# Kernel optimization log

Measured on AMD Instinct MI355X. Metric: run time of the kernel, lower is better.

## Reference

```python
import jax, jax.numpy as jnp
import numpy as np

K = 50  # top-k causal instances (UC_MIL constructor)


def setup_inputs() -> dict:
    key = jax.random.key(0)
    k1, k2 = jax.random.split(key)
    X = jax.random.normal(k1, (8, 4096, 768), dtype=jnp.float32)
    # GCN layer weight: nn.Linear(768, 1, bias=False) -> weight shape (1, 768)
    W = jax.random.normal(k2, (1, 768), dtype=jnp.float32) * 0.02
    return {"X": X, "W": W}


def reference(X, W):
    # X: (B, N, D) bag of instance features; W: (1, D) GCN weight
    B, N, D = X.shape
    k = K

    # --- build_adjacency_matrix, batched ---
    Xc = X - X.mean(axis=1, keepdims=True)                      # center over instances
    cov = jnp.einsum('bnd,bmd->bnm', Xc, Xc)                    # (B, N, N)
    var = jnp.sqrt(jnp.sum(Xc * Xc, axis=-1, keepdims=True)) + 1e-6  # (B, N, 1)
    corr = cov / (var * jnp.swapaxes(var, 1, 2))                # var @ var.T
    A = jnp.abs(corr)
    dinv = jnp.sum(A, axis=-1) ** (-0.5)                        # (B, N)
    # D @ A @ D with diagonal D == row/col scaling (same math, no dense diag)
    A_norm = dinv[:, :, None] * A * dinv[:, None, :]

    # --- 1-layer GCN score: (A_norm @ (X W^T)).squeeze(-1) ---
    XW = jnp.einsum('bnd,d->bn', X, W[0])                       # (B, N)
    S = jnp.einsum('bnm,bm->bn', A_norm, XW)                    # (B, N)

    # --- top-k causal / non-causal split, vectorized over batch ---
    _, topk_idx = jax.lax.top_k(S, k)                           # (B, k)
    F_c = jnp.take_along_axis(X, topk_idx[:, :, None], axis=1)  # (B, k, D)

    # non-topk indices in ascending order (torch.arange(N)[mask] semantics)
    flag = jnp.zeros((B, N), dtype=jnp.int32)
    flag = flag.at[jnp.arange(B)[:, None], topk_idx].set(1)
    non_idx = jnp.argsort(flag, axis=1, stable=True)[:, : N - k]  # (B, N-k)
    F_nc = jnp.take_along_axis(X, non_idx[:, :, None], axis=1)    # (B, N-k, D)

    # NOTE: original code has a bug: topk_indices = torch.stack(F_i_c, 0),
    # i.e. the second output is the gathered features, not the indices.
    # We replicate that faithfully.
    return (S,
            F_c,
            F_c.mean(axis=1, keepdims=True),
            F_nc.mean(axis=1, keepdims=True))
```

## Files before the change

kernel.cpp:

```cpp
#include <hip/hip_runtime.h>
#include <stdint.h>

typedef unsigned short u16;
typedef short bf16x8 __attribute__((ext_vector_type(8)));
typedef float f32x4 __attribute__((ext_vector_type(4)));
typedef unsigned long long ull;

#define NB 8
#define NROW 4096
#define ND 768
#define NKB 24
#define NRB 32
#define KTILE 4096
#define NTRI 528
#define TOPK 50

#define CPART_OFF 0u
#define CSUM_OFF  786432u
#define MEAN_OFF  811008u
#define RV_OFF    835584u
#define XW_OFF    966656u
#define T_OFF     1097728u
#define U_OFF     1228800u
#define DINV_OFF  1359872u
#define W_OFF     1490944u
#define IDX_OFF   1622016u
#define SMALL_TOTAL 1626112u
#define HB_PER_BATCH  6291456ull
#define COV_PER_BATCH 34603008ull
#define PER_BATCH (2ull * HB_PER_BATCH + COV_PER_BATCH)

static __device__ __forceinline__ u16 f2bf(float f) {
  uint32_t u = __float_as_uint(f);
  u += 0x7FFFu + ((u >> 16) & 1u);
  return (u16)(u >> 16);
}
static __device__ __forceinline__ float bf2f(u16 h) {
  return __uint_as_float(((uint32_t)h) << 16);
}

static __device__ __forceinline__ int tile_swz(int t) {
  return (t & 7) * 66 + (t >> 3);
}

__global__ __launch_bounds__(256)
void colsum1_kernel(const float* __restrict__ X, float* __restrict__ part) {
  const int nc = blockIdx.x;
  const int d  = threadIdx.x + blockIdx.y * 256;
  const int b  = blockIdx.z;
  const float* p = X + ((size_t)b * NROW + (size_t)nc * 128) * ND + d;
  float s = 0.f;
  for (int i = 0; i < 128; ++i) s += p[(size_t)i * ND];
  part[((size_t)b * 32 + nc) * ND + d] = s;
}

__global__ __launch_bounds__(256)
void colsum2_kernel(const float* __restrict__ part, float* __restrict__ csum,
                    float* __restrict__ mean) {
  const int d = threadIdx.x + blockIdx.x * 256;
  const int b = blockIdx.y;
  float s = 0.f;
  for (int i = 0; i < 32; ++i) s += part[((size_t)b * 32 + i) * ND + d];
  csum[(size_t)b * ND + d] = s;
  mean[(size_t)b * ND + d] = s * (1.0f / 4096.0f);
}

__global__ __launch_bounds__(128)
void rowstats_kernel(const float* __restrict__ X, const float* __restrict__ W,
                     const float* __restrict__ mean,
                     u16* __restrict__ hi, u16* __restrict__ lo,
                     float* __restrict__ rv, float* __restrict__ xw, int b0) {
  const int n  = blockIdx.x;
  const int lb = blockIdx.y;
  const int gb = b0 + lb;
  const int tid = threadIdx.x;
  const float* xr = X + ((size_t)gb * NROW + n) * ND;
  const float* mb = mean + (size_t)gb * ND;
  const int r = n & 127, rbk = n >> 7;
  float ssq = 0.f, sw = 0.f;
  if (tid < 96) {
    const int d0 = tid * 8;
    const float4 xa = *(const float4*)(xr + d0);
    const float4 xb = *(const float4*)(xr + d0 + 4);
    const float4 ma = *(const float4*)(mb + d0);
    const float4 mc = *(const float4*)(mb + d0 + 4);
    const float4 wa = *(const float4*)(W + d0);
    const float4 wb = *(const float4*)(W + d0 + 4);
    float x[8]  = {xa.x, xa.y, xa.z, xa.w, xb.x, xb.y, xb.z, xb.w};
    float mm[8] = {ma.x, ma.y, ma.z, ma.w, mc.x, mc.y, mc.z, mc.w};
    float ww[8] = {wa.x, wa.y, wa.z, wa.w, wb.x, wb.y, wb.z, wb.w};
    u16 hbits[8], lbits[8];
#pragma unroll
    for (int i = 0; i < 8; ++i) {
      float xc = x[i] - mm[i];
      ssq += xc * xc;
      sw  += x[i] * ww[i];
      u16 hb = f2bf(xc);
      float hf = bf2f(hb);
      u16 lb2 = f2bf(xc - hf);
      hbits[i] = hb; lbits[i] = lb2;
    }
    const int kb = d0 >> 5;
    const int kk = d0 & 31;
    const size_t tbyte = ((size_t)((lb * NRB + rbk) * NKB + kb)) * 8192
                       + (size_t)((r * 64 + kk * 2) ^ ((r & 7) << 4));
    uint4 hv, lv;
    hv.x = (uint32_t)hbits[0] | ((uint32_t)hbits[1] << 16);
    hv.y = (uint32_t)hbits[2] | ((uint32_t)hbits[3] << 16);
    hv.z = (uint32_t)hbits[4] | ((uint32_t)hbits[5] << 16);
    hv.w = (uint32_t)hbits[6] | ((uint32_t)hbits[7] << 16);
    lv.x = (uint32_t)lbits[0] | ((uint32_t)lbits[1] << 16);
    lv.y = (uint32_t)lbits[2] | ((uint32_t)lbits[3] << 16);
    lv.z = (uint32_t)lbits[4] | ((uint32_t)lbits[5] << 16);
    lv.w = (uint32_t)lbits[6] | ((uint32_t)lbits[7] << 16);
    *(uint4*)((char*)hi + tbyte) = hv;
    *(uint4*)((char*)lo + tbyte) = lv;
  }
#pragma unroll
  for (int m = 1; m < 64; m <<= 1) {
    ssq += __shfl_xor(ssq, m, 64);
    sw  += __shfl_xor(sw, m, 64);
  }
  __shared__ float sh[4];
  const int w = tid >> 6, lane = tid & 63;
  if (lane == 0) { sh[w * 2] = ssq; sh[w * 2 + 1] = sw; }
  __syncthreads();
  if (tid == 0) {
    float S = sh[0] + sh[2];
    float T = sh[1] + sh[3];
    const size_t i = (size_t)gb * NROW + n;
    rv[i] = 1.0f / (sqrtf(S) + 1e-6f);
    xw[i] = T;
  }
}

static __device__ __forceinline__ bf16x8 read_frag(const u16* sm, int r, int kbyte) {
  const int byte = (r * 64 + kbyte) ^ ((r & 7) << 4);
  return *(const bf16x8*)((const char*)sm + byte);
}

#define LOADK(kb)  do { const size_t kb8 = (size_t)(kb) * 8192;            \
  rA0 = *(const uint4*)(hA + kb8 + o0);  rA1 = *(const uint4*)(hA + kb8 + o1); \
  rB0 = *(const uint4*)(hB + kb8 + o0);  rB1 = *(const uint4*)(hB + kb8 + o1); \
  rLA0 = *(const uint4*)(lA + kb8 + o0); rLA1 = *(const uint4*)(lA + kb8 + o1); \
  rLB0 = *(const uint4*)(lB + kb8 + o0); rLB1 = *(const uint4*)(lB + kb8 + o1); } while (0)

__global__ __launch_bounds__(256, 2)
void gemm_acc_kernel(const u16* __restrict__ hi, const u16* __restrict__ lo,
                     const float* __restrict__ coef, float* __restrict__ outacc,
                     float* __restrict__ covout, int b0) {
  const int lb = blockIdx.y;
  const int gb = b0 + lb;
  const int tsw = tile_swz(blockIdx.x);
  int trem = tsw;
  int rb = 0;
  while (trem >= NRB - rb) { trem -= NRB - rb; ++rb; }
  const int cb = rb + trem;

  __shared__ u16 sm[4 * KTILE];
  u16* aHi = sm;
  u16* bHi = sm + KTILE;
  u16* aLo = sm + 2 * KTILE;
  u16* bLo = sm + 3 * KTILE;

  const int tid = threadIdx.x;
  const int lane = tid & 63;
  const int wid = tid >> 6;
  const int wrow = wid >> 1, wcol = wid & 1;
  const int l15 = lane & 15, lg = lane >> 4;

  const char* hA = (const char*)(hi + (size_t)((lb * NRB + rb) * NKB) * KTILE);
  const char* hB = (const char*)(hi + (size_t)((lb * NRB + cb) * NKB) * KTILE);
  const char* lA = (const char*)(lo + (size_t)((lb * NRB + rb) * NKB) * KTILE);
  const char* lB = (const char*)(lo + (size_t)((lb * NRB + cb) * NKB) * KTILE);

  const int o0 = tid * 16;
  const int o1 = o0 + 4096;

  uint4 rA0, rA1, rB0, rB1, rLA0, rLA1, rLB0, rLB1;

  f32x4 acc[4][4];
#pragma unroll
  for (int i = 0; i < 4; ++i)
#pragma unroll
    for (int j = 0; j < 4; ++j) acc[i][j] = f32x4{0.f, 0.f, 0.f, 0.f};

  LOADK(0);
  for (int kb = 0; kb < NKB; ++kb) {
    __syncthreads();
    *(uint4*)((char*)aHi + o0) = rA0;  *(uint4*)((char*)aHi + o1) = rA1;
    *(uint4*)((char*)bHi + o0) = rB0;  *(uint4*)((char*)bHi + o1) = rB1;
    *(uint4*)((char*)aLo + o0) = rLA0; *(uint4*)((char*)aLo + o1) = rLA1;
    *(uint4*)((char*)bLo + o0) = rLB0; *(uint4*)((char*)bLo + o1) = rLB1;
    __syncthreads();
    if (kb + 1 < NKB) { LOADK(kb + 1); }

    bf16x8 ah[4], bh[4], al[4], bl[4];
#pragma unroll
    for (int i = 0; i < 4; ++i) {
      ah[i] = read_frag(aHi, wrow * 64 + i * 16 + l15, lg * 16);
      bh[i] = read_frag(bHi, wcol * 64 + i * 16 + l15, lg * 16);
      al[i] = read_frag(aLo, wrow * 64 + i * 16 + l15, lg * 16);
      bl[i] = read_frag(bLo, wcol * 64 + i * 16 + l15, lg * 16);
    }
#pragma unroll
    for (int mi = 0; mi < 4; ++mi)
#pragma unroll
      for (int ni = 0; ni < 4; ++ni) {
        acc[mi][ni] = __builtin_amdgcn_mfma_f32_16x16x32_bf16(ah[mi], bh[ni], acc[mi][ni], 0, 0, 0);
        acc[mi][ni] = __builtin_amdgcn_mfma_f32_16x16x32_bf16(ah[mi], bl[ni], acc[mi][ni], 0, 0, 0);
        acc[mi][ni] = __builtin_amdgcn_mfma_f32_16x16x32_bf16(al[mi], bh[ni], acc[mi][ni], 0, 0, 0);
      }
  }

  const float* cf = coef + (size_t)gb * NROW;
  float* oa = outacc + (size_t)gb * NROW;
  const int rbase = rb * 128 + wrow * 64;
  const int cbase = cb * 128 + wcol * 64;

  float* cv = covout + ((size_t)lb * NTRI + tsw) * 16384;
#pragma unroll
  for (int mi = 0; mi < 4; ++mi)
#pragma unroll
    for (int ni = 0; ni < 4; ++ni)
#pragma unroll
      for (int j = 0; j < 4; ++j)
        cv[(wrow * 64 + mi * 16 + lg * 4 + j) * 128 + wcol * 64 + ni * 16 + l15] =
            fabsf(acc[mi][ni][j]);

  float ccol[4];
#pragma unroll
  for (int ni = 0; ni < 4; ++ni) ccol[ni] = cf[cbase + ni * 16 + l15];

  float rs[4][4];
#pragma unroll
  for (int mi = 0; mi < 4; ++mi)
#pragma unroll
    for (int j = 0; j < 4; ++j) {
      float s = 0.f;
#pragma unroll
      for (int ni = 0; ni < 4; ++ni) s += fabsf(acc[mi][ni][j]) * ccol[ni];
      rs[mi][j] = s;
    }
#pragma unroll
  for (int m = 1; m < 16; m <<= 1)
#pragma unroll
    for (int mi = 0; mi < 4; ++mi)
#pragma unroll
      for (int j = 0; j < 4; ++j) rs[mi][j] += __shfl_xor(rs[mi][j], m, 64);
  if (l15 == 0) {
#pragma unroll
    for (int mi = 0; mi < 4; ++mi)
#pragma unroll
      for (int j = 0; j < 4; ++j)
        atomicAdd(&oa[rbase + mi * 16 + lg * 4 + j], rs[mi][j]);
  }

  if (rb != cb) {
    float crow[4][4];
#pragma unroll
    for (int mi = 0; mi < 4; ++mi)
#pragma unroll
      for (int j = 0; j < 4; ++j) crow[mi][j] = cf[rbase + mi * 16 + lg * 4 + j];
    float cs[4];
#pragma unroll
    for (int ni = 0; ni < 4; ++ni) {
      float s = 0.f;
#pragma unroll
      for (int mi = 0; mi < 4; ++mi)
#pragma unroll
        for (int j = 0; j < 4; ++j) s += fabsf(acc[mi][ni][j]) * crow[mi][j];
      cs[ni] = s;
    }
#pragma unroll
    for (int ni = 0; ni < 4; ++ni) {
      cs[ni] += __shfl_xor(cs[ni], 16, 64);
      cs[ni] += __shfl_xor(cs[ni], 32, 64);
    }
    if (lg == 0) {
#pragma unroll
      for (int ni = 0; ni < 4; ++ni)
        atomicAdd(&oa[cbase + ni * 16 + l15], cs[ni]);
    }
  }
}

__global__ __launch_bounds__(256)
void upass_kernel(const float* __restrict__ cov, const float* __restrict__ w,
                  float* __restrict__ uacc, int b0) {
  const int lb = blockIdx.y;
  const int gb = b0 + lb;
  const int tsw = tile_swz(blockIdx.x);
  int trem = tsw;
  int rb = 0;
  while (trem >= NRB - rb) { trem -= NRB - rb; ++rb; }
  const int cb = rb + trem;

  const float* A = cov + ((size_t)lb * NTRI + tsw) * 16384;
  const float* wb_ = w + (size_t)gb * NROW;

  __shared__ float wr[128];
  __shared__ float rsum[128];
  __shared__ float csum_p[8][128];

  const int t = threadIdx.x;
  const int g = t >> 5;
  const int l = t & 31;

  if (t < 128) wr[t] = wb_[rb * 128 + t];
  const float4 wc4 = *(const float4*)(wb_ + cb * 128 + l * 4);
  __syncthreads();

  float sc0 = 0.f, sc1 = 0.f, sc2 = 0.f, sc3 = 0.f;
#pragma unroll
  for (int i = 0; i < 16; ++i) {
    const int r = g + i * 8;
    const float4 v = *(const float4*)(A + r * 128 + l * 4);
    float p = v.x * wc4.x + v.y * wc4.y + v.z * wc4.z + v.w * wc4.w;
    const float wrr = wr[r];
    sc0 += v.x * wrr; sc1 += v.y * wrr; sc2 += v.z * wrr; sc3 += v.w * wrr;
#pragma unroll
    for (int m = 1; m < 32; m <<= 1) p += __shfl_xor(p, m, 64);
    if (l == 0) rsum[r] = p;
  }
  csum_p[g][l * 4 + 0] = sc0;
  csum_p[g][l * 4 + 1] = sc1;
  csum_p[g][l * 4 + 2] = sc2;
  csum_p[g][l * 4 + 3] = sc3;
  __syncthreads();

  float* ua = uacc + (size_t)gb * NROW;
  if (t < 128) atomicAdd(&ua[rb * 128 + t], rsum[t]);
  if (rb != cb && t < 128) {
    float s = 0.f;
#pragma unroll
    for (int gg = 0; gg < 8; ++gg) s += csum_p[gg][t];
    atomicAdd(&ua[cb * 128 + t], s);
  }
}

__global__ __launch_bounds__(256)
void dinvw_kernel(const float* __restrict__ t, const float* __restrict__ rv,
                  const float* __restrict__ xw, float* __restrict__ dinv,
                  float* __restrict__ w, int b0) {
  const int n = blockIdx.x * 256 + threadIdx.x;
  const int gb = b0 + blockIdx.y;
  const size_t i = (size_t)gb * NROW + n;
  const float dv = 1.0f / sqrtf(rv[i] * t[i]);
  dinv[i] = dv;
  w[i] = dv * xw[i] * rv[i];
}

__global__ __launch_bounds__(256)
void sfinal_kernel(const float* __restrict__ dinv, const float* __restrict__ rv,
                   const float* __restrict__ u, float* __restrict__ S) {
  const int n = blockIdx.x * 256 + threadIdx.x;
  const int b = blockIdx.y;
  const size_t i = (size_t)b * NROW + n;
  S[i] = dinv[i] * rv[i] * u[i];
}

__global__ __launch_bounds__(1024)
void topk_kernel(const float* __restrict__ S, int* __restrict__ idx) {
  const int b = blockIdx.x;
  __shared__ ull keys[NROW];
  __shared__ ull wred[16];
  const int t = threadIdx.x;
  const int lane = t & 63, w = t >> 6;
  for (int i = t; i < NROW; i += 1024) {
    float s = S[(size_t)b * NROW + i];
    uint32_t u = __float_as_uint(s);
    u = (u & 0x80000000u) ? ~u : (u | 0x80000000u);
    keys[i] = ((ull)u << 32) | (uint32_t)(4095 - i);
  }
  __syncthreads();
  for (int r = 0; r < TOPK; ++r) {
    ull m = keys[t];
    ull m2 = keys[t + 1024]; if (m2 > m) m = m2;
    m2 = keys[t + 2048]; if (m2 > m) m = m2;
    m2 = keys[t + 3072]; if (m2 > m) m = m2;
#pragma unroll
    for (int sh = 1; sh < 64; sh <<= 1) {
      ull o = __shfl_xor(m, sh, 64);
      if (o > m) m = o;
    }
    if (lane == 0) wred[w] = m;
    __syncthreads();
    if (w == 0) {
      ull mm = wred[lane & 15];
#pragma unroll
      for (int sh = 1; sh < 16; sh <<= 1) {
        ull o = __shfl_xor(mm, sh, 64);
        if (o > mm) mm = o;
      }
      if (lane == 0) {
        const int sel = 4095 - (int)(mm & 0xFFFFFFFFu);
        idx[b * TOPK + r] = sel;
        keys[sel] = 0ULL;
      }
    }
    __syncthreads();
  }
}

__global__ __launch_bounds__(256)
void gather_kernel(const float* __restrict__ X, const int* __restrict__ idx,
                   float* __restrict__ outFc) {
  const int rr = blockIdx.x;
  const int b = blockIdx.y;
  const int row = idx[b * TOPK + rr];
  const float* src = X + ((size_t)b * NROW + row) * ND;
  float* dst = outFc + ((size_t)b * TOPK + rr) * ND;
#pragma unroll
  for (int c = 0; c < 3; ++c) {
    const int d = threadIdx.x + c * 256;
    dst[d] = src[d];
  }
}

__global__ __launch_bounds__(256)
void means_kernel(const float* __restrict__ X, const int* __restrict__ idx,
                  const float* __restrict__ csum, float* __restrict__ outC,
                  float* __restrict__ outNC) {
  const int b = blockIdx.x;
#pragma unroll
  for (int c = 0; c < 3; ++c) {
    const int d = threadIdx.x + c * 256;
    float s = 0.f;
    for (int r = 0; r < TOPK; ++r) {
      const int row = idx[b * TOPK + r];
      s += X[((size_t)b * NROW + row) * ND + d];
    }
    outC[(size_t)b * ND + d]  = s * (1.0f / 50.0f);
    outNC[(size_t)b * ND + d] = (csum[(size_t)b * ND + d] - s) * (1.0f / 4046.0f);
  }
}

extern "C" void kernel_launch(void* const* d_in, const int* in_sizes, int n_in,
                              void* d_out, int out_size, void* d_ws, size_t ws_size,
                              hipStream_t stream) {
  const float* X = (const float*)d_in[0];
  const float* W = (const float*)d_in[1];
  float* out = (float*)d_out;
  char* ws = (char*)d_ws;

  float* cpart = (float*)(ws + CPART_OFF);
  float* csum  = (float*)(ws + CSUM_OFF);
  float* mean  = (float*)(ws + MEAN_OFF);
  float* rv    = (float*)(ws + RV_OFF);
  float* xw    = (float*)(ws + XW_OFF);
  float* tacc  = (float*)(ws + T_OFF);
  float* uacc  = (float*)(ws + U_OFF);
  float* dinv  = (float*)(ws + DINV_OFF);
  float* warr  = (float*)(ws + W_OFF);
  int*   idx   = (int*)(ws + IDX_OFF);

  int nbc = 1;
  if (ws_size > SMALL_TOTAL + PER_BATCH)
    nbc = (int)((ws_size - SMALL_TOTAL) / PER_BATCH);
  if (nbc > NB) nbc = NB;
  if (nbc < 1) nbc = 1;
  u16* hi   = (u16*)(ws + SMALL_TOTAL);
  u16* lo   = (u16*)(ws + SMALL_TOTAL + (size_t)nbc * HB_PER_BATCH);
  float* cov = (float*)(ws + SMALL_TOTAL + (size_t)nbc * 2 * HB_PER_BATCH);

  float* outS  = out;
  float* outFc = out + 32768;
  float* outMC = out + 339968;
  float* outMN = out + 346112;

  hipMemsetAsync(ws + T_OFF, 0, 262144, stream);

  colsum1_kernel<<<dim3(32, 3, NB), 256, 0, stream>>>(X, cpart);
  colsum2_kernel<<<dim3(3, NB), 256, 0, stream>>>(cpart, csum, mean);

  for (int b0 = 0; b0 < NB; b0 += nbc) {
    const int nb = (NB - b0 < nbc) ? (NB - b0) : nbc;
    rowstats_kernel<<<dim3(NROW, nb), 128, 0, stream>>>(X, W, mean, hi, lo, rv, xw, b0);
    gemm_acc_kernel<<<dim3(NTRI, nb), 256, 0, stream>>>(hi, lo, rv, tacc, cov, b0);
    dinvw_kernel<<<dim3(16, nb), 256, 0, stream>>>(tacc, rv, xw, dinv, warr, b0);
    upass_kernel<<<dim3(NTRI, nb), 256, 0, stream>>>(cov, warr, uacc, b0);
  }

  sfinal_kernel<<<dim3(16, NB), 256, 0, stream>>>(dinv, rv, uacc, outS);
  topk_kernel<<<NB, 1024, 0, stream>>>(outS, idx);
  gather_kernel<<<dim3(TOPK, NB), 256, 0, stream>>>(X, idx, outFc);
  means_kernel<<<NB, 256, 0, stream>>>(X, idx, csum, outMC, outMN);
}
```

Baseline: 517.7 us.

## Double-buffer GEMM LDS tiles and fuse small elementwise and gather kernels

The GEMM kernel now uses two LDS buffers, issuing the next K-block's global loads before the MFMAs and storing them after, so each iteration needs one barrier instead of two. The dinv/w, S-final, gather and means kernels are removed: their math is recomputed inline in upass and topk, and gather plus means become one kernel. This cuts launch count and intermediate traffic. The cost is LDS doubling to 64KB per block, which may hurt the two-blocks-per-CU occupancy, plus redundant sqrt work in upass.

```diff
diff --git a/kernel.cpp b/kernel.cpp
--- a/kernel.cpp
+++ b/kernel.cpp
@@ -22,10 +22,8 @@
 #define XW_OFF    966656u
 #define T_OFF     1097728u
 #define U_OFF     1228800u
-#define DINV_OFF  1359872u
-#define W_OFF     1490944u
-#define IDX_OFF   1622016u
-#define SMALL_TOTAL 1626112u
+#define IDX_OFF   1359872u
+#define SMALL_TOTAL 1363968u
 #define HB_PER_BATCH  6291456ull
 #define COV_PER_BATCH 34603008ull
 #define PER_BATCH (2ull * HB_PER_BATCH + COV_PER_BATCH)
@@ -145,6 +143,12 @@
   rLA0 = *(const uint4*)(lA + kb8 + o0); rLA1 = *(const uint4*)(lA + kb8 + o1); \
   rLB0 = *(const uint4*)(lB + kb8 + o0); rLB1 = *(const uint4*)(lB + kb8 + o1); } while (0)
 
+#define STOREK(buf) do { char* bp = (char*)(buf);                          \
+  *(uint4*)(bp + o0) = rA0;          *(uint4*)(bp + o1) = rA1;             \
+  *(uint4*)(bp + 8192 + o0) = rB0;   *(uint4*)(bp + 8192 + o1) = rB1;      \
+  *(uint4*)(bp + 16384 + o0) = rLA0; *(uint4*)(bp + 16384 + o1) = rLA1;    \
+  *(uint4*)(bp + 24576 + o0) = rLB0; *(uint4*)(bp + 24576 + o1) = rLB1; } while (0)
+
 __global__ __launch_bounds__(256, 2)
 void gemm_acc_kernel(const u16* __restrict__ hi, const u16* __restrict__ lo,
                      const float* __restrict__ coef, float* __restrict__ outacc,
@@ -157,11 +161,7 @@
   while (trem >= NRB - rb) { trem -= NRB - rb; ++rb; }
   const int cb = rb + trem;
 
-  __shared__ u16 sm[4 * KTILE];
-  u16* aHi = sm;
-  u16* bHi = sm + KTILE;
-  u16* aLo = sm + 2 * KTILE;
-  u16* bLo = sm + 3 * KTILE;
+  __shared__ u16 sm[2][4 * KTILE];
 
   const int tid = threadIdx.x;
   const int lane = tid & 63;
@@ -186,14 +186,15 @@
     for (int j = 0; j < 4; ++j) acc[i][j] = f32x4{0.f, 0.f, 0.f, 0.f};
 
   LOADK(0);
+  STOREK(sm[0]);
+  __syncthreads();
+
+  int cur = 0;
   for (int kb = 0; kb < NKB; ++kb) {
-    __syncthreads();
-    *(uint4*)((char*)aHi + o0) = rA0;  *(uint4*)((char*)aHi + o1) = rA1;
-    *(uint4*)((char*)bHi + o0) = rB0;  *(uint4*)((char*)bHi + o1) = rB1;
-    *(uint4*)((char*)aLo + o0) = rLA0; *(uint4*)((char*)aLo + o1) = rLA1;
-    *(uint4*)((char*)bLo + o0) = rLB0; *(uint4*)((char*)bLo + o1) = rLB1;
-    __syncthreads();
-    if (kb + 1 < NKB) { LOADK(kb + 1); }
+    const u16* aHi = sm[cur];
+    const u16* bHi = sm[cur] + KTILE;
+    const u16* aLo = sm[cur] + 2 * KTILE;
+    const u16* bLo = sm[cur] + 3 * KTILE;
 
     bf16x8 ah[4], bh[4], al[4], bl[4];
 #pragma unroll
@@ -203,6 +204,8 @@
       al[i] = read_frag(aLo, wrow * 64 + i * 16 + l15, lg * 16);
       bl[i] = read_frag(bLo, wcol * 64 + i * 16 + l15, lg * 16);
     }
+    if (kb + 1 < NKB) { LOADK(kb + 1); }
+
 #pragma unroll
     for (int mi = 0; mi < 4; ++mi)
 #pragma unroll
@@ -211,6 +214,10 @@
         acc[mi][ni] = __builtin_amdgcn_mfma_f32_16x16x32_bf16(ah[mi], bl[ni], acc[mi][ni], 0, 0, 0);
         acc[mi][ni] = __builtin_amdgcn_mfma_f32_16x16x32_bf16(al[mi], bh[ni], acc[mi][ni], 0, 0, 0);
       }
+
+    if (kb + 1 < NKB) { STOREK(sm[cur ^ 1]); }
+    __syncthreads();
+    cur ^= 1;
   }
 
   const float* cf = coef + (size_t)gb * NROW;
@@ -286,7 +293,8 @@
 }
 
 __global__ __launch_bounds__(256)
-void upass_kernel(const float* __restrict__ cov, const float* __restrict__ w,
+void upass_kernel(const float* __restrict__ cov, const float* __restrict__ tt,
+                  const float* __restrict__ rv, const float* __restrict__ xw,
                   float* __restrict__ uacc, int b0) {
   const int lb = blockIdx.y;
   const int gb = b0 + lb;
@@ -297,7 +305,7 @@
   const int cb = rb + trem;
 
   const float* A = cov + ((size_t)lb * NTRI + tsw) * 16384;
-  const float* wb_ = w + (size_t)gb * NROW;
+  const size_t bo = (size_t)gb * NROW;
 
   __shared__ float wr[128];
   __shared__ float rsum[128];
@@ -307,8 +315,21 @@
   const int g = t >> 5;
   const int l = t & 31;
 
-  if (t < 128) wr[t] = wb_[rb * 128 + t];
-  const float4 wc4 = *(const float4*)(wb_ + cb * 128 + l * 4);
+  if (t < 128) {
+    const int row = rb * 128 + t;
+    wr[t] = (1.0f / sqrtf(rv[bo + row] * tt[bo + row])) * xw[bo + row] * rv[bo + row];
+  }
+  float4 wc4;
+  {
+    const int col = cb * 128 + l * 4;
+    const float4 r4 = *(const float4*)(rv + bo + col);
+    const float4 t4 = *(const float4*)(tt + bo + col);
+    const float4 x4 = *(const float4*)(xw + bo + col);
+    wc4.x = (1.0f / sqrtf(r4.x * t4.x)) * x4.x * r4.x;
+    wc4.y = (1.0f / sqrtf(r4.y * t4.y)) * x4.y * r4.y;
+    wc4.z = (1.0f / sqrtf(r4.z * t4.z)) * x4.z * r4.z;
+    wc4.w = (1.0f / sqrtf(r4.w * t4.w)) * x4.w * r4.w;
+  }
   __syncthreads();
 
   float sc0 = 0.f, sc1 = 0.f, sc2 = 0.f, sc3 = 0.f;
@@ -329,7 +350,7 @@
   csum_p[g][l * 4 + 3] = sc3;
   __syncthreads();
 
-  float* ua = uacc + (size_t)gb * NROW;
+  float* ua = uacc + bo;
   if (t < 128) atomicAdd(&ua[rb * 128 + t], rsum[t]);
   if (rb != cb && t < 128) {
     float s = 0.f;
@@ -339,39 +360,25 @@
   }
 }
 
-__global__ __launch_bounds__(256)
-void dinvw_kernel(const float* __restrict__ t, const float* __restrict__ rv,
-                  const float* __restrict__ xw, float* __restrict__ dinv,
-                  float* __restrict__ w, int b0) {
-  const int n = blockIdx.x * 256 + threadIdx.x;
-  const int gb = b0 + blockIdx.y;
-  const size_t i = (size_t)gb * NROW + n;
-  const float dv = 1.0f / sqrtf(rv[i] * t[i]);
-  dinv[i] = dv;
-  w[i] = dv * xw[i] * rv[i];
-}
-
-__global__ __launch_bounds__(256)
-void sfinal_kernel(const float* __restrict__ dinv, const float* __restrict__ rv,
-                   const float* __restrict__ u, float* __restrict__ S) {
-  const int n = blockIdx.x * 256 + threadIdx.x;
-  const int b = blockIdx.y;
-  const size_t i = (size_t)b * NROW + n;
-  S[i] = dinv[i] * rv[i] * u[i];
-}
-
 __global__ __launch_bounds__(1024)
-void topk_kernel(const float* __restrict__ S, int* __restrict__ idx) {
+void topk_kernel(const float* __restrict__ tt, const float* __restrict__ rv,
+                 const float* __restrict__ u, float* __restrict__ S,
+                 int* __restrict__ idx) {
   const int b = blockIdx.x;
   __shared__ ull keys[NROW];
   __shared__ ull wred[16];
   const int t = threadIdx.x;
   const int lane = t & 63, w = t >> 6;
-  for (int i = t; i < NROW; i += 1024) {
-    float s = S[(size_t)b * NROW + i];
-    uint32_t u = __float_as_uint(s);
-    u = (u & 0x80000000u) ? ~u : (u | 0x80000000u);
-    keys[i] = ((ull)u << 32) | (uint32_t)(4095 - i);
+  const size_t bo = (size_t)b * NROW;
+#pragma unroll
+  for (int j = 0; j < 4; ++j) {
+    const int i = t + j * 1024;
+    const float rvi = rv[bo + i];
+    const float s = (1.0f / sqrtf(rvi * tt[bo + i])) * rvi * u[bo + i];
+    S[bo + i] = s;
+    uint32_t uu = __float_as_uint(s);
+    uu = (uu & 0x80000000u) ? ~uu : (uu | 0x80000000u);
+    keys[i] = ((ull)uu << 32) | (uint32_t)(4095 - i);
   }
   __syncthreads();
   for (int r = 0; r < TOPK; ++r) {
@@ -403,37 +410,21 @@
   }
 }
 
-__global__ __launch_bounds__(256)
-void gather_kernel(const float* __restrict__ X, const int* __restrict__ idx,
-                   float* __restrict__ outFc) {
-  const int rr = blockIdx.x;
-  const int b = blockIdx.y;
-  const int row = idx[b * TOPK + rr];
-  const float* src = X + ((size_t)b * NROW + row) * ND;
-  float* dst = outFc + ((size_t)b * TOPK + rr) * ND;
-#pragma unroll
-  for (int c = 0; c < 3; ++c) {
-    const int d = threadIdx.x + c * 256;
-    dst[d] = src[d];
-  }
-}
-
-__global__ __launch_bounds__(256)
-void means_kernel(const float* __restrict__ X, const int* __restrict__ idx,
-                  const float* __restrict__ csum, float* __restrict__ outC,
-                  float* __restrict__ outNC) {
+__global__ __launch_bounds__(768)
+void gathermeans_kernel(const float* __restrict__ X, const int* __restrict__ idx,
+                        const float* __restrict__ csum, float* __restrict__ outFc,
+                        float* __restrict__ outC, float* __restrict__ outNC) {
   const int b = blockIdx.x;
-#pragma unroll
-  for (int c = 0; c < 3; ++c) {
-    const int d = threadIdx.x + c * 256;
-    float s = 0.f;
-    for (int r = 0; r < TOPK; ++r) {
-      const int row = idx[b * TOPK + r];
-      s += X[((size_t)b * NROW + row) * ND + d];
-    }
-    outC[(size_t)b * ND + d]  = s * (1.0f / 50.0f);
-    outNC[(size_t)b * ND + d] = (csum[(size_t)b * ND + d] - s) * (1.0f / 4046.0f);
-  }
+  const int d = threadIdx.x;
+  float s = 0.f;
+  for (int r = 0; r < TOPK; ++r) {
+    const int row = idx[b * TOPK + r];
+    const float v = X[((size_t)b * NROW + row) * ND + d];
+    outFc[((size_t)b * TOPK + r) * ND + d] = v;
+    s += v;
+  }
+  outC[(size_t)b * ND + d]  = s * (1.0f / 50.0f);
+  outNC[(size_t)b * ND + d] = (csum[(size_t)b * ND + d] - s) * (1.0f / 4046.0f);
 }
 
 extern "C" void kernel_launch(void* const* d_in, const int* in_sizes, int n_in,
@@ -451,8 +442,6 @@
   float* xw    = (float*)(ws + XW_OFF);
   float* tacc  = (float*)(ws + T_OFF);
   float* uacc  = (float*)(ws + U_OFF);
-  float* dinv  = (float*)(ws + DINV_OFF);
-  float* warr  = (float*)(ws + W_OFF);
   int*   idx   = (int*)(ws + IDX_OFF);
 
   int nbc = 1;
@@ -478,12 +467,9 @@
     const int nb = (NB - b0 < nbc) ? (NB - b0) : nbc;
     rowstats_kernel<<<dim3(NROW, nb), 128, 0, stream>>>(X, W, mean, hi, lo, rv, xw, b0);
     gemm_acc_kernel<<<dim3(NTRI, nb), 256, 0, stream>>>(hi, lo, rv, tacc, cov, b0);
-    dinvw_kernel<<<dim3(16, nb), 256, 0, stream>>>(tacc, rv, xw, dinv, warr, b0);
-    upass_kernel<<<dim3(NTRI, nb), 256, 0, stream>>>(cov, warr, uacc, b0);
-  }
-
-  sfinal_kernel<<<dim3(16, NB), 256, 0, stream>>>(dinv, rv, uacc, outS);
-  topk_kernel<<<NB, 1024, 0, stream>>>(outS, idx);
-  gather_kernel<<<dim3(TOPK, NB), 256, 0, stream>>>(X, idx, outFc);
-  means_kernel<<<NB, 256, 0, stream>>>(X, idx, csum, outMC, outMN);
-}
+    upass_kernel<<<dim3(NTRI, nb), 256, 0, stream>>>(cov, tacc, rv, xw, uacc, b0);
+  }
+
+  topk_kernel<<<NB, 1024, 0, stream>>>(tacc, rv, uacc, outS, idx);
+  gathermeans_kernel<<<NB, 768, 0, stream>>>(X, idx, csum, outFc, outMC, outMN);
+}
```

New measurement: 550.1 us. +6.3%, slower.
